# Performance work log

Hardware: AMD Instinct MI355X
Metric: run time of the kernel (lower is better)

The kernel has to match this reference:

```python
import jax, jax.numpy as jnp
import numpy as np

N, NFEAT, NHID, NHEADS, NCLASS = 4096, 64, 64, 4, 64
ALPHA = 0.2        # LeakyReLU negative slope
NEG = -9.0e15      # mask value from the torch code (-9e15)


def _xavier(key, shape, gain=1.414):
    fan_in, fan_out = shape[-2] if len(shape) > 1 else shape[-1], shape[-1]
    if len(shape) == 1:
        fan_in, fan_out = shape[0], 1
    bound = gain * np.sqrt(6.0 / (fan_in + fan_out))
    return jax.random.uniform(key, shape, jnp.float32, -bound, bound)


def setup_inputs() -> dict:
    key = jax.random.key(0)
    ks = jax.random.split(key, 6)
    x = jax.random.normal(ks[0], (N, NFEAT), jnp.float32)
    # sparse-ish adjacency mask with self loops (adj > 0 gating in torch code)
    adj = jax.random.bernoulli(ks[1], 0.02, (N, N)) | jnp.eye(N, dtype=bool)
    W_heads = _xavier(ks[2], (NHEADS, NFEAT, NHID))                  # per-head W
    a_heads = _xavier(ks[3], (NHEADS, 2 * NHID))                     # per-head a (flattened [2F',1])
    W_out = _xavier(ks[4], (NHEADS * NHID, NCLASS))
    a_out = _xavier(ks[5], (2 * NCLASS,))
    return {"x": x, "W_heads": W_heads, "a_heads": a_heads,
            "W_out": W_out, "a_out": a_out, "adj": adj}


def gat_layer(x, adj, W, a, concat):
    # h: [N, F']
    h = x @ W
    Fp = h.shape[-1]
    # e_ij = leakyrelu(a[:F'].h_i + a[F':].h_j)  == torch's cat([h_i, h_j]) @ a
    f1 = h @ a[:Fp]                 # [N]
    f2 = h @ a[Fp:]                 # [N]
    e = jax.nn.leaky_relu(f1[:, None] + f2[None, :], ALPHA)   # [N, N]
    att = jax.nn.softmax(jnp.where(adj, e, NEG), axis=1)      # row softmax over neighbors
    hp = att @ h                    # [N, F']
    return jax.nn.elu(hp) if concat else hp


def reference(x, W_heads, a_heads, W_out, a_out, adj):
    # multi-head GAT with concat (dropout omitted: eval mode)
    heads = jax.vmap(lambda W, a: gat_layer(x, adj, W, a, True))(W_heads, a_heads)  # [H, N, F']
    hcat = jnp.transpose(heads, (1, 0, 2)).reshape(x.shape[0], NHEADS * NHID)       # [N, H*F']
    out = gat_layer(hcat, adj, W_out, a_out, False)                                  # [N, nclass]
    return out
```

## Files before the change

### kernel.cpp

```cpp
#include <hip/hip_runtime.h>
#include <hip/hip_fp16.h>

#define N 4096
#define CAP 160
#define ALPHA 0.2f

__device__ __forceinline__ float wred_sum(float v) {
#pragma unroll
  for (int o = 32; o > 0; o >>= 1) v += __shfl_xor(v, o, 64);
  return v;
}

__device__ __forceinline__ void h8_fma(float4 raw, float p, float* acc) {
  union { float4 f4; __half2 h2[4]; } u;
  u.f4 = raw;
#pragma unroll
  for (int t = 0; t < 4; ++t) {
    float2 v = __half22float2(u.h2[t]);
    acc[2 * t]     = fmaf(p, v.x, acc[2 * t]);
    acc[2 * t + 1] = fmaf(p, v.y, acc[2 * t + 1]);
  }
}

__global__ void stage1_k(const void* __restrict__ adjv, const float* __restrict__ x,
                         const float* __restrict__ W, const float* __restrict__ a,
                         int* __restrict__ cnt, int* __restrict__ cols,
                         __half* __restrict__ h1, float* __restrict__ f1h,
                         float* __restrict__ f2h) {
  __shared__ float Ws[64 * 64];
  __shared__ float xs[4][64];
  __shared__ int csh;
  int bid = blockIdx.x;
  int tid = threadIdx.x;
  int lane = tid & 63;
  if (bid < N) {
    int i = bid;
    if (tid == 0) csh = 0;
    __syncthreads();
    int* mycols = cols + (size_t)i * CAP;
    const unsigned char* adjB = (const unsigned char*)adjv;
    bool byteLayout = (adjB[(size_t)N + 1] == 1);
    unsigned long long lt = (lane == 0) ? 0ull : (~0ull >> (64 - lane));
    if (!byteLayout) {
      const int4* row = (const int4*)((const int*)adjv + (size_t)i * N);
      int4 v[4];
#pragma unroll
      for (int it = 0; it < 4; ++it) v[it] = row[tid + it * 256];
#pragma unroll
      for (int it = 0; it < 4; ++it) {
        int b = (tid + it * 256) * 4;
        unsigned long long m0 = __ballot(v[it].x != 0);
        unsigned long long m1 = __ballot(v[it].y != 0);
        unsigned long long m2 = __ballot(v[it].z != 0);
        unsigned long long m3 = __ballot(v[it].w != 0);
        int c0 = __popcll(m0), c1 = __popcll(m1), c2 = __popcll(m2);
        int total = c0 + c1 + c2 + __popcll(m3);
        int wb = 0;
        if (lane == 0 && total) wb = atomicAdd(&csh, total);
        wb = __shfl(wb, 0, 64);
        if (v[it].x) { int p = wb + __popcll(m0 & lt); if (p < CAP) mycols[p] = b; }
        if (v[it].y) { int p = wb + c0 + __popcll(m1 & lt); if (p < CAP) mycols[p] = b + 1; }
        if (v[it].z) { int p = wb + c0 + c1 + __popcll(m2 & lt); if (p < CAP) mycols[p] = b + 2; }
        if (v[it].w) { int p = wb + c0 + c1 + c2 + __popcll(m3 & lt); if (p < CAP) mycols[p] = b + 3; }
      }
    } else {
      const uint4* row4 = (const uint4*)(adjB + (size_t)i * N);
      uint4 vv = row4[tid];
      unsigned int v[4] = {vv.x, vv.y, vv.z, vv.w};
#pragma unroll
      for (int it = 0; it < 4; ++it) {
        int b = tid * 16 + it * 4;
        unsigned long long m0 = __ballot((v[it] & 0xffu) != 0);
        unsigned long long m1 = __ballot((v[it] & 0xff00u) != 0);
        unsigned long long m2 = __ballot((v[it] & 0xff0000u) != 0);
        unsigned long long m3 = __ballot((v[it] & 0xff000000u) != 0);
        int c0 = __popcll(m0), c1 = __popcll(m1), c2 = __popcll(m2);
        int total = c0 + c1 + c2 + __popcll(m3);
        int wb = 0;
        if (lane == 0 && total) wb = atomicAdd(&csh, total);
        wb = __shfl(wb, 0, 64);
        if (v[it] & 0xffu) { int p = wb + __popcll(m0 & lt); if (p < CAP) mycols[p] = b; }
        if (v[it] & 0xff00u) { int p = wb + c0 + __popcll(m1 & lt); if (p < CAP) mycols[p] = b + 1; }
        if (v[it] & 0xff0000u) { int p = wb + c0 + c1 + __popcll(m2 & lt); if (p < CAP) mycols[p] = b + 2; }
        if (v[it] & 0xff000000u) { int p = wb + c0 + c1 + c2 + __popcll(m3 & lt); if (p < CAP) mycols[p] = b + 3; }
      }
    }
    __syncthreads();
    if (tid == 0) cnt[i] = min(csh, CAP);
  } else {
    int u = bid - N;
    int h = u & 3;
    int r = tid >> 6, f = lane;
    int n = (u >> 2) * 4 + r;
    const float4* W4 = (const float4*)(W + h * 4096);
    float4* Ws4 = (float4*)Ws;
    for (int t = tid; t < 1024; t += 256) Ws4[t] = W4[t];
    xs[r][f] = x[(size_t)n * 64 + f];
    __syncthreads();
    float acc = 0.f;
#pragma unroll
    for (int k = 0; k < 64; k += 4) {
      float4 xk = *(const float4*)&xs[r][k];
      acc = fmaf(xk.x, Ws[k * 64 + f], acc);
      acc = fmaf(xk.y, Ws[(k + 1) * 64 + f], acc);
      acc = fmaf(xk.z, Ws[(k + 2) * 64 + f], acc);
      acc = fmaf(xk.w, Ws[(k + 3) * 64 + f], acc);
    }
    h1[((size_t)h * N + n) * 64 + f] = __float2half(acc);
    float s1 = wred_sum(acc * a[h * 128 + f]);
    float s2 = wred_sum(acc * a[h * 128 + 64 + f]);
    if (f == 0) { f1h[n * 4 + h] = s1; f2h[n * 4 + h] = s2; }
  }
}

__global__ void attn1_gemm_k(const int* __restrict__ cnt, const int* __restrict__ cols,
                             const __half* __restrict__ h1,
                             const float* __restrict__ f1g,
                             const float* __restrict__ f2g,
                             const float* __restrict__ Wout,
                             const float* __restrict__ aout,
                             __half* __restrict__ h2, float* __restrict__ f1o,
                             float* __restrict__ f2o) {
  int i0 = blockIdx.x * 2;
  int i1 = i0 + 1;
  int tid = threadIdx.x;
  int w = tid >> 6, lane = tid & 63;
  __shared__ int cS[2][CAP];
  __shared__ float pS[2][4][CAP];
  __shared__ float red[4][2][4];
  __shared__ float sDinv[2][4];
  __shared__ float hrow[2][256];
  __shared__ float4 part4[2][4][16];
  int c0 = cnt[i0], c1 = cnt[i1];
  float4 t10 = ((const float4*)f1g)[i0];
  float4 t11 = ((const float4*)f1g)[i1];
  float f1r[2][4] = {{t10.x, t10.y, t10.z, t10.w}, {t11.x, t11.y, t11.z, t11.w}};
  float dloc[2][4] = {{0.f, 0.f, 0.f, 0.f}, {0.f, 0.f, 0.f, 0.f}};
#pragma unroll
  for (int rr = 0; rr < 2; ++rr) {
    int c = rr ? c1 : c0;
    int ii = rr ? i1 : i0;
    for (int k = tid; k < c; k += 256) {
      int j = cols[(size_t)ii * CAP + k];
      cS[rr][k] = j;
      float4 t2 = ((const float4*)f2g)[j];
      float f2v[4] = {t2.x, t2.y, t2.z, t2.w};
#pragma unroll
      for (int h = 0; h < 4; ++h) {
        float s = f1r[rr][h] + f2v[h];
        s = s > 0.f ? s : ALPHA * s;
        float p = __expf(s);
        pS[rr][h][k] = p;
        dloc[rr][h] += p;
      }
    }
  }
#pragma unroll
  for (int rr = 0; rr < 2; ++rr)
#pragma unroll
    for (int h = 0; h < 4; ++h) {
      float d = wred_sum(dloc[rr][h]);
      if (lane == 0) red[w][rr][h] = d;
    }
  __syncthreads();
  if (tid < 8) {
    int rr = tid >> 2, h = tid & 3;
    float d = red[0][rr][h] + red[1][rr][h] + red[2][rr][h] + red[3][rr][h];
    int c = rr ? c1 : c0;
    sDinv[rr][h] = (c > 0) ? 1.f / d : 0.f;
  }
  __syncthreads();
  int g = lane >> 3, ff = lane & 7, h = w;
  const __half* hb = h1 + ((size_t)h * N) * 64;
  float a0[8] = {0.f, 0.f, 0.f, 0.f, 0.f, 0.f, 0.f, 0.f};
  float a1[8] = {0.f, 0.f, 0.f, 0.f, 0.f, 0.f, 0.f, 0.f};
  int cmax = c0 > c1 ? c0 : c1;
#pragma unroll 2
  for (int k0 = 0; k0 < cmax; k0 += 8) {
    int k = k0 + g;
    bool o0 = k < c0, o1 = k < c1;
    int j0 = o0 ? cS[0][k] : 0, j1 = o1 ? cS[1][k] : 0;
    float p0 = o0 ? pS[0][h][k] : 0.f, p1 = o1 ? pS[1][h][k] : 0.f;
    float4 r0 = *(const float4*)(hb + (size_t)j0 * 64 + ff * 8);
    float4 r1 = *(const float4*)(hb + (size_t)j1 * 64 + ff * 8);
    h8_fma(r0, p0, a0);
    h8_fma(r1, p1, a1);
  }
#pragma unroll
  for (int o = 8; o < 64; o <<= 1)
#pragma unroll
    for (int e = 0; e < 8; ++e) {
      a0[e] += __shfl_xor(a0[e], o, 64);
      a1[e] += __shfl_xor(a1[e], o, 64);
    }
  if (g == 0) {
    float d0 = sDinv[0][h], d1 = sDinv[1][h];
#pragma unroll
    for (int e = 0; e < 8; ++e) {
      float v0 = a0[e] * d0;
      float v1 = a1[e] * d1;
      v0 = v0 > 0.f ? v0 : expm1f(v0);
      v1 = v1 > 0.f ? v1 : expm1f(v1);
      hrow[0][h * 64 + ff * 8 + e] = v0;
      hrow[1][h * 64 + ff * 8 + e] = v1;
    }
  }
  __syncthreads();
  int ko = lane >> 4, f4 = lane & 15;
  float4 wa0 = {0.f, 0.f, 0.f, 0.f}, wa1 = wa0;
#pragma unroll
  for (int kk = 0; kk < 64; kk += 4) {
    int k = w * 64 + kk + ko;
    float4 wv = *(const float4*)(Wout + (size_t)k * 64 + f4 * 4);
    float h0 = hrow[0][k], h1v = hrow[1][k];
    wa0.x = fmaf(h0, wv.x, wa0.x); wa0.y = fmaf(h0, wv.y, wa0.y);
    wa0.z = fmaf(h0, wv.z, wa0.z); wa0.w = fmaf(h0, wv.w, wa0.w);
    wa1.x = fmaf(h1v, wv.x, wa1.x); wa1.y = fmaf(h1v, wv.y, wa1.y);
    wa1.z = fmaf(h1v, wv.z, wa1.z); wa1.w = fmaf(h1v, wv.w, wa1.w);
  }
#pragma unroll
  for (int o = 16; o < 64; o <<= 1) {
    wa0.x += __shfl_xor(wa0.x, o, 64); wa0.y += __shfl_xor(wa0.y, o, 64);
    wa0.z += __shfl_xor(wa0.z, o, 64); wa0.w += __shfl_xor(wa0.w, o, 64);
    wa1.x += __shfl_xor(wa1.x, o, 64); wa1.y += __shfl_xor(wa1.y, o, 64);
    wa1.z += __shfl_xor(wa1.z, o, 64); wa1.w += __shfl_xor(wa1.w, o, 64);
  }
  if (ko == 0) { part4[0][w][f4] = wa0; part4[1][w][f4] = wa1; }
  __syncthreads();
  if (tid < 32) {
    int rr = tid >> 4, fi = tid & 15;
    float4 s0 = part4[rr][0][fi], s1_ = part4[rr][1][fi];
    float4 s2_ = part4[rr][2][fi], s3_ = part4[rr][3][fi];
    float4 s = {(s0.x + s1_.x) + (s2_.x + s3_.x), (s0.y + s1_.y) + (s2_.y + s3_.y),
                (s0.z + s1_.z) + (s2_.z + s3_.z), (s0.w + s1_.w) + (s2_.w + s3_.w)};
    int i = rr ? i1 : i0;
    __half2* dst = (__half2*)(h2 + (size_t)i * 64 + fi * 4);
    dst[0] = __floats2half2_rn(s.x, s.y);
    dst[1] = __floats2half2_rn(s.z, s.w);
    float4 aA = *(const float4*)(aout + fi * 4);
    float4 aB = *(const float4*)(aout + 64 + fi * 4);
    float s1 = s.x * aA.x + s.y * aA.y + s.z * aA.z + s.w * aA.w;
    float s2 = s.x * aB.x + s.y * aB.y + s.z * aB.z + s.w * aB.w;
#pragma unroll
    for (int o = 1; o < 16; o <<= 1) {
      s1 += __shfl_xor(s1, o, 64);
      s2 += __shfl_xor(s2, o, 64);
    }
    if (fi == 0) { f1o[i] = s1; f2o[i] = s2; }
  }
}

__global__ void attn2_k(const int* __restrict__ cnt, const int* __restrict__ cols,
                        const __half* __restrict__ h2,
                        const float* __restrict__ f1g,
                        const float* __restrict__ f2g,
                        float* __restrict__ outf) {
  int i = blockIdx.x;
  int tid = threadIdx.x;
  int w = tid >> 6, lane = tid & 63;
  __shared__ int cS[CAP];
  __shared__ float pS[CAP];
  __shared__ float red[4];
  __shared__ float sDinv;
  __shared__ float partF[4][64];
  int c = cnt[i];
  float f1i = f1g[i];
  float dloc = 0.f;
  for (int k = tid; k < c; k += 256) {
    int j = cols[(size_t)i * CAP + k];
    cS[k] = j;
    float s = f1i + f2g[j];
    s = s > 0.f ? s : ALPHA * s;
    float p = __expf(s);
    pS[k] = p;
    dloc += p;
  }
  float d = wred_sum(dloc);
  if (lane == 0) red[w] = d;
  __syncthreads();
  if (tid == 0) {
    float dd = red[0] + red[1] + red[2] + red[3];
    sDinv = (c > 0) ? 1.f / dd : 0.f;
  }
  __syncthreads();
  int g = lane >> 3, ff = lane & 7;
  float acc[8] = {0.f, 0.f, 0.f, 0.f, 0.f, 0.f, 0.f, 0.f};
#pragma unroll 2
  for (int k0 = 0; k0 < c; k0 += 32) {
    int k = k0 + w * 8 + g;
    bool o = k < c;
    int j = o ? cS[k] : 0;
    float p = o ? pS[k] : 0.f;
    float4 rv = *(const float4*)(h2 + (size_t)j * 64 + ff * 8);
    h8_fma(rv, p, acc);
  }
#pragma unroll
  for (int o = 8; o < 64; o <<= 1)
#pragma unroll
    for (int e = 0; e < 8; ++e) acc[e] += __shfl_xor(acc[e], o, 64);
  if (g == 0)
#pragma unroll
    for (int e = 0; e < 8; ++e) partF[w][ff * 8 + e] = acc[e];
  __syncthreads();
  if (tid < 64) {
    float v = (partF[0][tid] + partF[1][tid] + partF[2][tid] + partF[3][tid]) * sDinv;
    outf[(size_t)i * 64 + tid] = v;
  }
}

extern "C" void kernel_launch(void* const* d_in, const int* in_sizes, int n_in,
                              void* d_out, int out_size, void* d_ws, size_t ws_size,
                              hipStream_t stream) {
  const float* x    = (const float*)d_in[0];
  const float* Wh   = (const float*)d_in[1];
  const float* ah   = (const float*)d_in[2];
  const float* Wout = (const float*)d_in[3];
  const float* aout = (const float*)d_in[4];
  const void*  adj  = d_in[5];

  char* ws = (char*)d_ws;
  int* cnt  = (int*)ws;   ws += (size_t)N * sizeof(int);
  int* cols = (int*)ws;   ws += (size_t)N * CAP * sizeof(int);
  __half* h1 = (__half*)ws; ws += (size_t)N * 256 * sizeof(__half);
  float* f1h  = (float*)ws; ws += (size_t)N * 4 * sizeof(float);
  float* f2h  = (float*)ws; ws += (size_t)N * 4 * sizeof(float);
  __half* h2 = (__half*)ws; ws += (size_t)N * 64 * sizeof(__half);
  float* f1o  = (float*)ws; ws += (size_t)N * sizeof(float);
  float* f2o  = (float*)ws; ws += (size_t)N * sizeof(float);
  (void)in_sizes; (void)n_in; (void)out_size; (void)ws_size;

  stage1_k<<<2 * N, 256, 0, stream>>>(adj, x, Wh, ah, cnt, cols, h1, f1h, f2h);
  attn1_gemm_k<<<N / 2, 256, 0, stream>>>(cnt, cols, h1, f1h, f2h, Wout, aout,
                                          h2, f1o, f2o);
  attn2_k<<<N, 256, 0, stream>>>(cnt, cols, h2, f1o, f2o, (float*)d_out);
}
```

Before: 146.4 us.

## Tile stage1 GEMM to 16 rows per block and give each attn2 row one wavefront

The per-head projection GEMM blocks in stage1 now compute 16 rows each (4 per wavefront) instead of 4. This cuts the number of times the 16 KB W tile is reloaded from 4096 to 1024 blocks and places these blocks first in the grid. attn2 now assigns one wavefront per output row (4 rows per block), which removes the cross-wave shared-memory reduction and most of the block barriers, and it writes output with float4 stores. The trade-off is less parallelism per row in attn2, where each wave walks all neighbours alone, and a longer serial FMA chain per thread in the GEMM blocks.

```diff
diff --git a/kernel.cpp b/kernel.cpp
--- a/kernel.cpp
+++ b/kernel.cpp
@@ -4,6 +4,7 @@
 #define N 4096
 #define CAP 160
 #define ALPHA 0.2f
+#define NGEMM 1024
 
 __device__ __forceinline__ float wred_sum(float v) {
 #pragma unroll
@@ -28,13 +29,55 @@
                          __half* __restrict__ h1, float* __restrict__ f1h,
                          float* __restrict__ f2h) {
   __shared__ float Ws[64 * 64];
-  __shared__ float xs[4][64];
+  __shared__ float xs[16][64];
   __shared__ int csh;
   int bid = blockIdx.x;
   int tid = threadIdx.x;
   int lane = tid & 63;
-  if (bid < N) {
-    int i = bid;
+  if (bid < NGEMM) {
+    int u = bid;
+    int h = u & 3;
+    int rowbase = (u >> 2) * 16;
+    int r = tid >> 6, f = lane;
+    const float4* W4 = (const float4*)(W + h * 4096);
+    float4* Ws4 = (float4*)Ws;
+#pragma unroll
+    for (int t = 0; t < 4; ++t) Ws4[tid + t * 256] = W4[tid + t * 256];
+    ((float4*)xs)[tid] = ((const float4*)(x + (size_t)rowbase * 64))[tid];
+    __syncthreads();
+    int n0 = 4 * r;
+    float acc0 = 0.f, acc1 = 0.f, acc2 = 0.f, acc3 = 0.f;
+#pragma unroll
+    for (int k = 0; k < 64; k += 4) {
+      float w0 = Ws[k * 64 + f];
+      float w1 = Ws[(k + 1) * 64 + f];
+      float w2 = Ws[(k + 2) * 64 + f];
+      float w3 = Ws[(k + 3) * 64 + f];
+      float4 x0 = *(const float4*)&xs[n0 + 0][k];
+      float4 x1 = *(const float4*)&xs[n0 + 1][k];
+      float4 x2 = *(const float4*)&xs[n0 + 2][k];
+      float4 x3 = *(const float4*)&xs[n0 + 3][k];
+      acc0 = fmaf(x0.x, w0, acc0); acc0 = fmaf(x0.y, w1, acc0);
+      acc0 = fmaf(x0.z, w2, acc0); acc0 = fmaf(x0.w, w3, acc0);
+      acc1 = fmaf(x1.x, w0, acc1); acc1 = fmaf(x1.y, w1, acc1);
+      acc1 = fmaf(x1.z, w2, acc1); acc1 = fmaf(x1.w, w3, acc1);
+      acc2 = fmaf(x2.x, w0, acc2); acc2 = fmaf(x2.y, w1, acc2);
+      acc2 = fmaf(x2.z, w2, acc2); acc2 = fmaf(x2.w, w3, acc2);
+      acc3 = fmaf(x3.x, w0, acc3); acc3 = fmaf(x3.y, w1, acc3);
+      acc3 = fmaf(x3.z, w2, acc3); acc3 = fmaf(x3.w, w3, acc3);
+    }
+    float a1v = a[h * 128 + f], a2v = a[h * 128 + 64 + f];
+    float accv[4] = {acc0, acc1, acc2, acc3};
+#pragma unroll
+    for (int j = 0; j < 4; ++j) {
+      int n = rowbase + n0 + j;
+      h1[((size_t)h * N + n) * 64 + f] = __float2half(accv[j]);
+      float s1 = wred_sum(accv[j] * a1v);
+      float s2 = wred_sum(accv[j] * a2v);
+      if (f == 0) { f1h[n * 4 + h] = s1; f2h[n * 4 + h] = s2; }
+    }
+  } else {
+    int i = bid - NGEMM;
     if (tid == 0) csh = 0;
     __syncthreads();
     int* mycols = cols + (size_t)i * CAP;
@@ -87,29 +130,6 @@
     }
     __syncthreads();
     if (tid == 0) cnt[i] = min(csh, CAP);
-  } else {
-    int u = bid - N;
-    int h = u & 3;
-    int r = tid >> 6, f = lane;
-    int n = (u >> 2) * 4 + r;
-    const float4* W4 = (const float4*)(W + h * 4096);
-    float4* Ws4 = (float4*)Ws;
-    for (int t = tid; t < 1024; t += 256) Ws4[t] = W4[t];
-    xs[r][f] = x[(size_t)n * 64 + f];
-    __syncthreads();
-    float acc = 0.f;
-#pragma unroll
-    for (int k = 0; k < 64; k += 4) {
-      float4 xk = *(const float4*)&xs[r][k];
-      acc = fmaf(xk.x, Ws[k * 64 + f], acc);
-      acc = fmaf(xk.y, Ws[(k + 1) * 64 + f], acc);
-      acc = fmaf(xk.z, Ws[(k + 2) * 64 + f], acc);
-      acc = fmaf(xk.w, Ws[(k + 3) * 64 + f], acc);
-    }
-    h1[((size_t)h * N + n) * 64 + f] = __float2half(acc);
-    float s1 = wred_sum(acc * a[h * 128 + f]);
-    float s2 = wred_sum(acc * a[h * 128 + 64 + f]);
-    if (f == 0) { f1h[n * 4 + h] = s1; f2h[n * 4 + h] = s2; }
   }
 }
 
@@ -255,42 +275,34 @@
                         const float* __restrict__ f1g,
                         const float* __restrict__ f2g,
                         float* __restrict__ outf) {
-  int i = blockIdx.x;
   int tid = threadIdx.x;
   int w = tid >> 6, lane = tid & 63;
-  __shared__ int cS[CAP];
-  __shared__ float pS[CAP];
-  __shared__ float red[4];
-  __shared__ float sDinv;
-  __shared__ float partF[4][64];
+  int i = blockIdx.x * 4 + w;
+  __shared__ int cS[4][CAP];
+  __shared__ float pS[4][CAP];
   int c = cnt[i];
   float f1i = f1g[i];
   float dloc = 0.f;
-  for (int k = tid; k < c; k += 256) {
+  for (int k = lane; k < c; k += 64) {
     int j = cols[(size_t)i * CAP + k];
-    cS[k] = j;
+    cS[w][k] = j;
     float s = f1i + f2g[j];
     s = s > 0.f ? s : ALPHA * s;
     float p = __expf(s);
-    pS[k] = p;
+    pS[w][k] = p;
     dloc += p;
   }
-  float d = wred_sum(dloc);
-  if (lane == 0) red[w] = d;
-  __syncthreads();
-  if (tid == 0) {
-    float dd = red[0] + red[1] + red[2] + red[3];
-    sDinv = (c > 0) ? 1.f / dd : 0.f;
-  }
+  float dtot = wred_sum(dloc);
+  float dinv = (c > 0) ? 1.f / dtot : 0.f;
   __syncthreads();
   int g = lane >> 3, ff = lane & 7;
   float acc[8] = {0.f, 0.f, 0.f, 0.f, 0.f, 0.f, 0.f, 0.f};
 #pragma unroll 2
-  for (int k0 = 0; k0 < c; k0 += 32) {
-    int k = k0 + w * 8 + g;
+  for (int k0 = 0; k0 < c; k0 += 8) {
+    int k = k0 + g;
     bool o = k < c;
-    int j = o ? cS[k] : 0;
-    float p = o ? pS[k] : 0.f;
+    int j = o ? cS[w][k] : 0;
+    float p = o ? pS[w][k] : 0.f;
     float4 rv = *(const float4*)(h2 + (size_t)j * 64 + ff * 8);
     h8_fma(rv, p, acc);
   }
@@ -298,13 +310,12 @@
   for (int o = 8; o < 64; o <<= 1)
 #pragma unroll
     for (int e = 0; e < 8; ++e) acc[e] += __shfl_xor(acc[e], o, 64);
-  if (g == 0)
-#pragma unroll
-    for (int e = 0; e < 8; ++e) partF[w][ff * 8 + e] = acc[e];
-  __syncthreads();
-  if (tid < 64) {
-    float v = (partF[0][tid] + partF[1][tid] + partF[2][tid] + partF[3][tid]) * sDinv;
-    outf[(size_t)i * 64 + tid] = v;
+  if (g == 0) {
+    float4 v0 = {acc[0] * dinv, acc[1] * dinv, acc[2] * dinv, acc[3] * dinv};
+    float4 v1 = {acc[4] * dinv, acc[5] * dinv, acc[6] * dinv, acc[7] * dinv};
+    float* dst = outf + (size_t)i * 64 + ff * 8;
+    *(float4*)dst = v0;
+    *(float4*)(dst + 4) = v1;
   }
 }
 
@@ -329,8 +340,8 @@
   float* f2o  = (float*)ws; ws += (size_t)N * sizeof(float);
   (void)in_sizes; (void)n_in; (void)out_size; (void)ws_size;
 
-  stage1_k<<<2 * N, 256, 0, stream>>>(adj, x, Wh, ah, cnt, cols, h1, f1h, f2h);
+  stage1_k<<<NGEMM + N, 256, 0, stream>>>(adj, x, Wh, ah, cnt, cols, h1, f1h, f2h);
   attn1_gemm_k<<<N / 2, 256, 0, stream>>>(cnt, cols, h1, f1h, f2h, Wout, aout,
                                           h2, f1o, f2o);
-  attn2_k<<<N, 256, 0, stream>>>(cnt, cols, h2, f1o, f2o, (float*)d_out);
-}
+  attn2_k<<<N / 4, 256, 0, stream>>>(cnt, cols, h2, f1o, f2o, (float*)d_out);
+}
```

New measurement: 197.2 us. 1.35x slower.

## Process one output row per wavefront in the second attention kernel

Applied to the files above, without the earlier changes.

The final attention kernel now assigns one node row to each 64-lane wavefront, packing four rows per 256-thread block, instead of spreading a single row across the whole block. This removes the block-wide __syncthreads barriers and the cross-wave shared-memory reductions for the softmax denominator and the output features. Output stores are vectorized as float4 from the reducing lanes. In exchange each wavefront runs more serial iterations over its neighbor list, and rows with different neighbor counts now share a block, so load balance within a block may be uneven.

```diff
diff --git a/kernel.cpp b/kernel.cpp
--- a/kernel.cpp
+++ b/kernel.cpp
@@ -255,42 +255,33 @@
                         const float* __restrict__ f1g,
                         const float* __restrict__ f2g,
                         float* __restrict__ outf) {
-  int i = blockIdx.x;
   int tid = threadIdx.x;
   int w = tid >> 6, lane = tid & 63;
-  __shared__ int cS[CAP];
-  __shared__ float pS[CAP];
-  __shared__ float red[4];
-  __shared__ float sDinv;
-  __shared__ float partF[4][64];
+  int i = blockIdx.x * 4 + w;
+  __shared__ int cS[4][CAP];
+  __shared__ float pS[4][CAP];
   int c = cnt[i];
   float f1i = f1g[i];
   float dloc = 0.f;
-  for (int k = tid; k < c; k += 256) {
+  for (int k = lane; k < c; k += 64) {
     int j = cols[(size_t)i * CAP + k];
-    cS[k] = j;
+    cS[w][k] = j;
     float s = f1i + f2g[j];
     s = s > 0.f ? s : ALPHA * s;
     float p = __expf(s);
-    pS[k] = p;
+    pS[w][k] = p;
     dloc += p;
   }
-  float d = wred_sum(dloc);
-  if (lane == 0) red[w] = d;
-  __syncthreads();
-  if (tid == 0) {
-    float dd = red[0] + red[1] + red[2] + red[3];
-    sDinv = (c > 0) ? 1.f / dd : 0.f;
-  }
-  __syncthreads();
+  float dtot = wred_sum(dloc);
+  float dinv = (c > 0) ? 1.f / dtot : 0.f;
   int g = lane >> 3, ff = lane & 7;
   float acc[8] = {0.f, 0.f, 0.f, 0.f, 0.f, 0.f, 0.f, 0.f};
 #pragma unroll 2
-  for (int k0 = 0; k0 < c; k0 += 32) {
-    int k = k0 + w * 8 + g;
+  for (int k0 = 0; k0 < c; k0 += 8) {
+    int k = k0 + g;
     bool o = k < c;
-    int j = o ? cS[k] : 0;
-    float p = o ? pS[k] : 0.f;
+    int j = o ? cS[w][k] : 0;
+    float p = o ? pS[w][k] : 0.f;
     float4 rv = *(const float4*)(h2 + (size_t)j * 64 + ff * 8);
     h8_fma(rv, p, acc);
   }
@@ -298,13 +289,12 @@
   for (int o = 8; o < 64; o <<= 1)
 #pragma unroll
     for (int e = 0; e < 8; ++e) acc[e] += __shfl_xor(acc[e], o, 64);
-  if (g == 0)
-#pragma unroll
-    for (int e = 0; e < 8; ++e) partF[w][ff * 8 + e] = acc[e];
-  __syncthreads();
-  if (tid < 64) {
-    float v = (partF[0][tid] + partF[1][tid] + partF[2][tid] + partF[3][tid]) * sDinv;
-    outf[(size_t)i * 64 + tid] = v;
+  if (g == 0) {
+    float4 v0 = {acc[0] * dinv, acc[1] * dinv, acc[2] * dinv, acc[3] * dinv};
+    float4 v1 = {acc[4] * dinv, acc[5] * dinv, acc[6] * dinv, acc[7] * dinv};
+    float* dst = outf + (size_t)i * 64 + ff * 8;
+    *(float4*)dst = v0;
+    *(float4*)(dst + 4) = v1;
   }
 }
 
@@ -332,5 +322,5 @@
   stage1_k<<<2 * N, 256, 0, stream>>>(adj, x, Wh, ah, cnt, cols, h1, f1h, f2h);
   attn1_gemm_k<<<N / 2, 256, 0, stream>>>(cnt, cols, h1, f1h, f2h, Wout, aout,
                                           h2, f1o, f2o);
-  attn2_k<<<N, 256, 0, stream>>>(cnt, cols, h2, f1o, f2o, (float*)d_out);
-}
+  attn2_k<<<N / 4, 256, 0, stream>>>(cnt, cols, h2, f1o, f2o, (float*)d_out);
+}
```

Result: faster. 142.7 us (-2.5%).
